# Kernel optimization log

Measured on AMD Instinct MI355X. Metric: run time of the kernel, lower is better.

The kernel has to match this reference:

```python
import jax, jax.numpy as jnp
import numpy as np

B = 256      # number of graphs
IN = 128     # input_dim
FD = 256     # feature_dim (dims[1])
HID = 256    # hidden_dim of attention block (dims[2])
OUT = 128    # final output dim (dims[3])
TXT = 512    # text_emb_dim

LENGTHS = np.asarray(128 + (np.arange(B) % 256), dtype=np.int64)  # ragged lens 128..383
N = int(LENGTHS.sum())  # 65408 total nodes
LMAX = int(LENGTHS.max())  # 383


def setup_inputs() -> dict:
    key = jax.random.key(0)
    ks = jax.random.split(key, 16)
    s = 0.02
    return {
        "input": jax.random.normal(ks[0], (N, IN), jnp.float32),
        "text_emb": jax.random.normal(ks[1], (B, TXT), jnp.float32),
        "repeat_list": jnp.asarray(LENGTHS),
        # layer 0: Linear(IN -> FD)
        "W0": jax.random.normal(ks[2], (IN, FD), jnp.float32) * s,
        "b0": jax.random.normal(ks[3], (FD,), jnp.float32) * s,
        # cross-attention block params
        "Wq": jax.random.normal(ks[4], (TXT, FD), jnp.float32) * s,
        "bq": jax.random.normal(ks[5], (FD,), jnp.float32) * s,
        "Wk": jax.random.normal(ks[6], (FD, FD), jnp.float32) * s,
        "bk": jax.random.normal(ks[7], (FD,), jnp.float32) * s,
        "Wv": jax.random.normal(ks[8], (FD, FD), jnp.float32) * s,
        "bv": jax.random.normal(ks[9], (FD,), jnp.float32) * s,
        "Wo": jax.random.normal(ks[10], (FD, HID), jnp.float32) * s,
        "bo": jax.random.normal(ks[11], (HID,), jnp.float32) * s,
        # layer 2: Linear(HID -> OUT), last layer (no activation)
        "W2": jax.random.normal(ks[12], (HID, OUT), jnp.float32) * s,
        "b2": jax.random.normal(ks[13], (OUT,), jnp.float32) * s,
    }


def _cross_attention(h, text_emb, repeat_list, Wq, bq, Wk, bk, Wv, bv, Wo, bo):
    # h: [N, FD] packed ragged node features; repeat_list: [B] lengths (constant ints)
    n = h.shape[0]
    b = repeat_list.shape[0]
    fd = h.shape[1]
    # pad ragged -> [B, LMAX, FD] (pad value 0) + validity mask
    seg = jnp.repeat(jnp.arange(b), repeat_list, total_repeat_length=n)  # [N] graph id
    offsets = jnp.cumsum(repeat_list) - repeat_list                      # [B] start of each graph
    pos = jnp.arange(n) - offsets[seg]                                   # [N] within-graph pos
    padded = jnp.zeros((b, LMAX, fd), h.dtype).at[seg, pos].set(h)
    valid = jnp.arange(LMAX)[None, :] < repeat_list[:, None]             # [B, L]

    q = text_emb @ Wq + bq                              # [B, FD]
    k = (padded @ Wk + bk) * valid[..., None]           # masked_fill(mask==0, 0)
    v = (padded @ Wv + bv) * valid[..., None]

    # query is broadcast identically over the padded-length axis, so each row of the
    # [L, L] score matrix is the same vector: scores[b, j] = q[b] . k[b, j]
    scores = jnp.einsum('bf,bjf->bj', q, k)             # [B, L]
    scores = jnp.where(valid, scores, -jnp.inf)         # mask invalid columns j
    p = jax.nn.softmax(scores, axis=-1)                 # [B, L]
    # output = attention^T @ value with identical rows => out[b,j,:] = p[b,j] * sum_i v[b,i,:]
    v_sum = v.sum(axis=1)                               # [B, FD] (padded rows already zero)
    out_pad = p[..., None] * v_sum[:, None, :]          # [B, L, FD]
    out_nodes = out_pad[seg, pos]                       # unpad-concat -> [N, FD]
    return out_nodes @ Wo + bo                          # [N, HID]


def reference(input, text_emb, repeat_list, W0, b0, Wq, bq, Wk, bk, Wv, bv, Wo, bo, W2, b2):
    h = jax.nn.relu(input @ W0 + b0)                                     # layer 0 + relu
    h = _cross_attention(h, text_emb, repeat_list, Wq, bq, Wk, bk, Wv, bv, Wo, bo)
    h = jax.nn.relu(h)                                                   # layer 1 + relu
    return h @ W2 + b2                                                   # layer 2 (last, no act)
```

## Files before the change

kernel.cpp:

```cpp
#include <hip/hip_runtime.h>
#include <math.h>

#define B_G   256
#define IN_D  128
#define FD    256
#define HID   256
#define OUT_D 128
#define TXT   512

typedef short bf16x8 __attribute__((ext_vector_type(8)));
typedef float f32x4  __attribute__((ext_vector_type(4)));

__device__ __forceinline__ unsigned bf_rne(float x) {
    unsigned u = __float_as_uint(x);
    u += 0x7fffu + ((u >> 16) & 1u);
    return u >> 16;
}
__device__ __forceinline__ float bf_to_f(unsigned h) {
    return __uint_as_float(h << 16);
}
__device__ __forceinline__ void split2(float a0, float a1, unsigned& hp, unsigned& lp) {
    unsigned h0 = bf_rne(a0), h1 = bf_rne(a1);
    float r0 = a0 - bf_to_f(h0), r1 = a1 - bf_to_f(h1);
    hp = h0 | (h1 << 16);
    lp = bf_rne(r0) | (bf_rne(r1) << 16);
}
__device__ __forceinline__ void split8(const float* z, bf16x8& hf, bf16x8& lf) {
    uint4 h, l;
    split2(z[0], z[1], h.x, l.x);
    split2(z[2], z[3], h.y, l.y);
    split2(z[4], z[5], h.z, l.z);
    split2(z[6], z[7], h.w, l.w);
    hf = __builtin_bit_cast(bf16x8, h);
    lf = __builtin_bit_cast(bf16x8, l);
}

__global__ __launch_bounds__(256) void k_prepA(
    const float* __restrict__ text_emb, const float* __restrict__ Wq,
    const float* __restrict__ bq, const float* __restrict__ Wk,
    const float* __restrict__ W0, const float* __restrict__ W2,
    const int* __restrict__ lens,
    float* __restrict__ qk, int* __restrict__ offsets, float* __restrict__ hsum,
    unsigned short* __restrict__ W0sH, unsigned short* __restrict__ W0sL,
    unsigned short* __restrict__ W2sH, unsigned short* __restrict__ W2sL)
{
    int blk = blockIdx.x, t = threadIdx.x;
    __shared__ float te[TXT];
    __shared__ float q[FD];
    __shared__ int   sc[B_G];

    if (blk < 256) {
        int b = blk;
        hsum[b * FD + t] = 0.f;
        for (int i = t; i < TXT; i += 256) te[i] = text_emb[(size_t)b * TXT + i];
        __syncthreads();
        float acc = bq[t];
        for (int k = 0; k < TXT; k++) acc = fmaf(te[k], Wq[k * FD + t], acc);
        q[t] = acc;
        __syncthreads();
        float a2 = 0.f;
        for (int f = 0; f < FD; f++) a2 = fmaf(Wk[t * FD + f], q[f], a2);
        qk[b * FD + t] = a2;
    } else if (blk < 264) {
        int e = (blk - 256) * 256 + t;
        if (e < 1024) {
            int kc = e >> 8, c = e & 255;
            size_t base = (size_t)(kc * 256 + c) * 32;
            for (int kk = 0; kk < 32; kk++) {
                float v = W0[(size_t)(kc * 32 + kk) * FD + c];
                unsigned h = bf_rne(v);
                float r = v - bf_to_f(h);
                W0sH[base + kk] = (unsigned short)h;
                W0sL[base + kk] = (unsigned short)bf_rne(r);
            }
        } else {
            int e2 = e - 1024;
            int kc = e2 >> 7, c = e2 & 127;
            size_t base = (size_t)(kc * 128 + c) * 32;
            for (int kk = 0; kk < 32; kk++) {
                float v = W2[(size_t)(kc * 32 + kk) * OUT_D + c];
                unsigned h = bf_rne(v);
                float r = v - bf_to_f(h);
                W2sH[base + kk] = (unsigned short)h;
                W2sL[base + kk] = (unsigned short)bf_rne(r);
            }
        }
    } else {
        sc[t] = lens[t];
        __syncthreads();
        for (int d = 1; d < 256; d <<= 1) {
            int v = (t >= d) ? sc[t - d] : 0;
            __syncthreads();
            sc[t] += v;
            __syncthreads();
        }
        offsets[t + 1] = sc[t];
        if (t == 0) offsets[0] = 0;
    }
}

__global__ __launch_bounds__(256, 2) void k_l0_mfma(
    const float* __restrict__ X,
    const unsigned short* __restrict__ W0sH, const unsigned short* __restrict__ W0sL,
    const float* __restrict__ b0, const float* __restrict__ qk,
    const int* __restrict__ offsets,
    float* __restrict__ scores, float* __restrict__ hsum)
{
    int b = blockIdx.y;
    int off = offsets[b], len = offsets[b + 1] - off;
    int n0 = blockIdx.x * 64;
    if (n0 >= len) return;
    int nvalid = min(64, len - n0);

    __shared__ float qks[FD];
    __shared__ float bsh[FD];
    __shared__ float red[4][64];

    int tid = threadIdx.x;
    int lane = tid & 63, w = tid >> 6;
    int ln = lane & 15, quad = lane >> 4;

    qks[tid] = qk[b * FD + tid];
    bsh[tid] = b0[tid];

    const float* Xbase = X + (size_t)(off + n0) * IN_D;

    f32x4 acc[4][4] = {};
#pragma unroll
    for (int kc = 0; kc < 4; kc++) {
        bf16x8 AH[4], AL[4], BH[4], BL[4];
#pragma unroll
        for (int i = 0; i < 4; i++) {
            int node = 16 * i + ln;
            float xv[8];
            if (node < nvalid) {
                const float4* p = (const float4*)(Xbase + (size_t)node * IN_D + kc * 32 + quad * 8);
                float4 v0 = p[0], v1 = p[1];
                xv[0] = v0.x; xv[1] = v0.y; xv[2] = v0.z; xv[3] = v0.w;
                xv[4] = v1.x; xv[5] = v1.y; xv[6] = v1.z; xv[7] = v1.w;
            } else {
#pragma unroll
                for (int q2 = 0; q2 < 8; q2++) xv[q2] = 0.f;
            }
            split8(xv, AH[i], AL[i]);
        }
#pragma unroll
        for (int j = 0; j < 4; j++) {
            int c = 64 * w + 16 * j + ln;
            size_t base = (size_t)(kc * 256 + c) * 32 + quad * 8;
            BH[j] = *(const bf16x8*)&W0sH[base];
            BL[j] = *(const bf16x8*)&W0sL[base];
        }
#pragma unroll
        for (int i = 0; i < 4; i++)
#pragma unroll
            for (int j = 0; j < 4; j++) {
                acc[i][j] = __builtin_amdgcn_mfma_f32_16x16x32_bf16(AH[i], BH[j], acc[i][j], 0, 0, 0);
                acc[i][j] = __builtin_amdgcn_mfma_f32_16x16x32_bf16(AH[i], BL[j], acc[i][j], 0, 0, 0);
                acc[i][j] = __builtin_amdgcn_mfma_f32_16x16x32_bf16(AL[i], BH[j], acc[i][j], 0, 0, 0);
            }
    }
    __syncthreads();

    float sp[4][4];
    float cs[4] = {0.f, 0.f, 0.f, 0.f};
#pragma unroll
    for (int i = 0; i < 4; i++)
#pragma unroll
        for (int r = 0; r < 4; r++) sp[i][r] = 0.f;

#pragma unroll
    for (int i = 0; i < 4; i++)
#pragma unroll
        for (int j = 0; j < 4; j++) {
            int c = 64 * w + 16 * j + ln;
            float bb = bsh[c], qv = qks[c];
#pragma unroll
            for (int r = 0; r < 4; r++) {
                int node = 16 * i + 4 * quad + r;
                float h = acc[i][j][r] + bb;
                h = (h > 0.f && node < nvalid) ? h : 0.f;
                sp[i][r] = fmaf(h, qv, sp[i][r]);
                cs[j] += h;
            }
        }
#pragma unroll
    for (int i = 0; i < 4; i++)
#pragma unroll
        for (int r = 0; r < 4; r++) {
            float s = sp[i][r];
            s += __shfl_xor(s, 1); s += __shfl_xor(s, 2);
            s += __shfl_xor(s, 4); s += __shfl_xor(s, 8);
            sp[i][r] = s;
        }
    if (ln == 0) {
#pragma unroll
        for (int i = 0; i < 4; i++)
#pragma unroll
            for (int r = 0; r < 4; r++)
                red[w][16 * i + 4 * quad + r] = sp[i][r];
    }
#pragma unroll
    for (int j = 0; j < 4; j++) {
        float s = cs[j];
        s += __shfl_xor(s, 16); s += __shfl_xor(s, 32);
        if (quad == 0) atomicAdd(&hsum[b * FD + 64 * w + 16 * j + ln], s);
    }
    __syncthreads();
    if (tid < 64 && tid < nvalid)
        scores[off + n0 + tid] = red[0][tid] + red[1][tid] + red[2][tid] + red[3][tid];
}

__global__ __launch_bounds__(1024) void k_graph(
    const float* __restrict__ scores, const float* __restrict__ hsum,
    const float* __restrict__ Wv, const float* __restrict__ bv,
    const float* __restrict__ Wo, const int* __restrict__ offsets,
    float* __restrict__ wvec, float* __restrict__ smax, float* __restrict__ dinv)
{
    int b = blockIdx.x, tid = threadIdx.x;
    int t = tid & 255, g = tid >> 8;
    int off = offsets[b], len = offsets[b + 1] - off;
    __shared__ float redm[16], reds[16];
    __shared__ float hs[FD], vs[FD];
    __shared__ float part[4][FD];

    float m = -INFINITY;
    for (int i = tid; i < len; i += 1024) m = fmaxf(m, scores[off + i]);
    for (int d = 1; d < 64; d <<= 1) m = fmaxf(m, __shfl_xor(m, d));
    if ((tid & 63) == 0) redm[tid >> 6] = m;
    __syncthreads();
    m = -INFINITY;
#pragma unroll
    for (int k = 0; k < 16; k++) m = fmaxf(m, redm[k]);

    float s = 0.f;
    for (int i = tid; i < len; i += 1024) s += expf(scores[off + i] - m);
    for (int d = 1; d < 64; d <<= 1) s += __shfl_xor(s, d);
    if ((tid & 63) == 0) reds[tid >> 6] = s;
    if (g == 0) hs[t] = hsum[b * FD + t];
    __syncthreads();
    s = 0.f;
#pragma unroll
    for (int k = 0; k < 16; k++) s += reds[k];

    float acc = (g == 0) ? (float)len * bv[t] : 0.f;
    for (int f = 64 * g; f < 64 * g + 64; f++) acc = fmaf(hs[f], Wv[f * FD + t], acc);
    part[g][t] = acc;
    __syncthreads();
    if (g == 0) vs[t] = part[0][t] + part[1][t] + part[2][t] + part[3][t];
    __syncthreads();
    float a2 = 0.f;
    for (int f = 64 * g; f < 64 * g + 64; f++) a2 = fmaf(vs[f], Wo[f * HID + t], a2);
    part[g][t] = a2;
    __syncthreads();
    if (g == 0) wvec[b * HID + t] = part[0][t] + part[1][t] + part[2][t] + part[3][t];
    if (tid == 0) { smax[b] = m; dinv[b] = 1.0f / s; }
}

__global__ __launch_bounds__(256, 2) void k_fin_mfma(
    const float* __restrict__ scores, const float* __restrict__ wvec,
    const float* __restrict__ bo,
    const unsigned short* __restrict__ W2sH, const unsigned short* __restrict__ W2sL,
    const float* __restrict__ b2, const float* __restrict__ smax,
    const float* __restrict__ dinv, const int* __restrict__ offsets,
    float* __restrict__ Y)
{
    int b = blockIdx.y;
    int off = offsets[b], len = offsets[b + 1] - off;
    int n0 = blockIdx.x * 64;
    if (n0 >= len) return;
    int nvalid = min(64, len - n0);

    int tid = threadIdx.x;
    int lane = tid & 63, w = tid >> 6;
    int ln = lane & 15, quad = lane >> 4;

    __shared__ float wsh[HID];
    __shared__ float bosh[HID];
    __shared__ float b2sh[OUT_D];

    wsh[tid] = wvec[b * HID + tid];
    bosh[tid] = bo[tid];
    if (tid < OUT_D) b2sh[tid] = b2[tid];

    float sm = smax[b], di = dinv[b];
    float p[4];
#pragma unroll
    for (int i = 0; i < 4; i++) {
        int node = 16 * i + ln;
        p[i] = (node < nvalid) ? expf(scores[off + n0 + node] - sm) * di : 0.f;
    }
    __syncthreads();

    f32x4 acc[4][2] = {};
#pragma unroll
    for (int kc = 0; kc < 8; kc++) {
        float wv[8], bov[8];
        {
            const float4* wp = (const float4*)&wsh[kc * 32 + quad * 8];
            const float4* bp = (const float4*)&bosh[kc * 32 + quad * 8];
            float4 w0 = wp[0], w1 = wp[1], c0 = bp[0], c1 = bp[1];
            wv[0] = w0.x; wv[1] = w0.y; wv[2] = w0.z; wv[3] = w0.w;
            wv[4] = w1.x; wv[5] = w1.y; wv[6] = w1.z; wv[7] = w1.w;
            bov[0] = c0.x; bov[1] = c0.y; bov[2] = c0.z; bov[3] = c0.w;
            bov[4] = c1.x; bov[5] = c1.y; bov[6] = c1.z; bov[7] = c1.w;
        }
        bf16x8 AH[4], AL[4], BH[2], BL[2];
#pragma unroll
        for (int i = 0; i < 4; i++) {
            float z[8];
#pragma unroll
            for (int jj = 0; jj < 8; jj++)
                z[jj] = fmaxf(fmaf(p[i], wv[jj], bov[jj]), 0.f);
            split8(z, AH[i], AL[i]);
        }
#pragma unroll
        for (int j = 0; j < 2; j++) {
            int c = 32 * w + 16 * j + ln;
            size_t base = (size_t)(kc * 128 + c) * 32 + quad * 8;
            BH[j] = *(const bf16x8*)&W2sH[base];
            BL[j] = *(const bf16x8*)&W2sL[base];
        }
#pragma unroll
        for (int i = 0; i < 4; i++)
#pragma unroll
            for (int j = 0; j < 2; j++) {
                acc[i][j] = __builtin_amdgcn_mfma_f32_16x16x32_bf16(AH[i], BH[j], acc[i][j], 0, 0, 0);
                acc[i][j] = __builtin_amdgcn_mfma_f32_16x16x32_bf16(AH[i], BL[j], acc[i][j], 0, 0, 0);
                acc[i][j] = __builtin_amdgcn_mfma_f32_16x16x32_bf16(AL[i], BH[j], acc[i][j], 0, 0, 0);
            }
    }

#pragma unroll
    for (int i = 0; i < 4; i++)
#pragma unroll
        for (int j = 0; j < 2; j++) {
            int c = 32 * w + 16 * j + ln;
            float bb = b2sh[c];
#pragma unroll
            for (int r = 0; r < 4; r++) {
                int node = 16 * i + 4 * quad + r;
                if (node < nvalid)
                    Y[(size_t)(off + n0 + node) * OUT_D + c] = acc[i][j][r] + bb;
            }
        }
}

extern "C" void kernel_launch(void* const* d_in, const int* in_sizes, int n_in,
                              void* d_out, int out_size, void* d_ws, size_t ws_size,
                              hipStream_t stream)
{
    const float* X        = (const float*)d_in[0];
    const float* text_emb = (const float*)d_in[1];
    const int*   lens     = (const int*)d_in[2];
    const float* W0       = (const float*)d_in[3];
    const float* b0       = (const float*)d_in[4];
    const float* Wq       = (const float*)d_in[5];
    const float* bq       = (const float*)d_in[6];
    const float* Wk       = (const float*)d_in[7];
    const float* Wv       = (const float*)d_in[9];
    const float* bv       = (const float*)d_in[10];
    const float* Wo       = (const float*)d_in[11];
    const float* bo       = (const float*)d_in[12];
    const float* W2       = (const float*)d_in[13];
    const float* b2       = (const float*)d_in[14];
    float* Y = (float*)d_out;

    char* base = (char*)d_ws;
    size_t o = 0;
    int*   offsets = (int*)(base + o);            o += 1088;
    float* qkbuf   = (float*)(base + o);          o += 262144;
    float* wvec    = (float*)(base + o);          o += 262144;
    float* smaxb   = (float*)(base + o);          o += 1024;
    float* dinvb   = (float*)(base + o);          o += 1024;
    float* hsum    = (float*)(base + o);          o += 262144;
    float* scores  = (float*)(base + o);          o += 262144;
    unsigned short* W0sH = (unsigned short*)(base + o); o += 65536;
    unsigned short* W0sL = (unsigned short*)(base + o); o += 65536;
    unsigned short* W2sH = (unsigned short*)(base + o); o += 65536;
    unsigned short* W2sL = (unsigned short*)(base + o); o += 65536;

    k_prepA<<<265, 256, 0, stream>>>(text_emb, Wq, bq, Wk, W0, W2, lens,
                                     qkbuf, offsets, hsum, W0sH, W0sL, W2sH, W2sL);
    k_l0_mfma<<<dim3(6, B_G), 256, 0, stream>>>(X, W0sH, W0sL, b0, qkbuf, offsets, scores, hsum);
    k_graph<<<B_G, 1024, 0, stream>>>(scores, hsum, Wv, bv, Wo, offsets, wvec, smaxb, dinvb);
    k_fin_mfma<<<dim3(6, B_G), 256, 0, stream>>>(scores, wvec, bo, W2sH, W2sL, b2, smaxb, dinvb, offsets, Y);
}
```

Before: 210.4 us.

## Drop activation low-part MFMA, prefetch operands, and widen prep kernel blocks

The activation operand in both MFMA GEMMs is no longer split into bf16 high and low parts, which cuts the MFMA count per tile from three to two. Weights still use the split, so accuracy falls to roughly bf16 rounding of activations. The next k-chunk's X rows and W2 fragments are now loaded into registers ahead of use to overlap load latency with compute. The prep kernel moves to 1024-thread blocks that split the q and qk dot products four ways, giving more parallelism per graph at the cost of an extra shared-memory reduction.

```diff
diff --git a/kernel.cpp b/kernel.cpp
--- a/kernel.cpp
+++ b/kernel.cpp
@@ -19,23 +19,16 @@
 __device__ __forceinline__ float bf_to_f(unsigned h) {
     return __uint_as_float(h << 16);
 }
-__device__ __forceinline__ void split2(float a0, float a1, unsigned& hp, unsigned& lp) {
-    unsigned h0 = bf_rne(a0), h1 = bf_rne(a1);
-    float r0 = a0 - bf_to_f(h0), r1 = a1 - bf_to_f(h1);
-    hp = h0 | (h1 << 16);
-    lp = bf_rne(r0) | (bf_rne(r1) << 16);
-}
-__device__ __forceinline__ void split8(const float* z, bf16x8& hf, bf16x8& lf) {
-    uint4 h, l;
-    split2(z[0], z[1], h.x, l.x);
-    split2(z[2], z[3], h.y, l.y);
-    split2(z[4], z[5], h.z, l.z);
-    split2(z[6], z[7], h.w, l.w);
-    hf = __builtin_bit_cast(bf16x8, h);
-    lf = __builtin_bit_cast(bf16x8, l);
-}
-
-__global__ __launch_bounds__(256) void k_prepA(
+__device__ __forceinline__ bf16x8 pack_hi8(const float4& v0, const float4& v1) {
+    uint4 h;
+    h.x = bf_rne(v0.x) | (bf_rne(v0.y) << 16);
+    h.y = bf_rne(v0.z) | (bf_rne(v0.w) << 16);
+    h.z = bf_rne(v1.x) | (bf_rne(v1.y) << 16);
+    h.w = bf_rne(v1.z) | (bf_rne(v1.w) << 16);
+    return __builtin_bit_cast(bf16x8, h);
+}
+
+__global__ __launch_bounds__(1024) void k_prepA(
     const float* __restrict__ text_emb, const float* __restrict__ Wq,
     const float* __restrict__ bq, const float* __restrict__ Wk,
     const float* __restrict__ W0, const float* __restrict__ W2,
@@ -44,25 +37,32 @@
     unsigned short* __restrict__ W0sH, unsigned short* __restrict__ W0sL,
     unsigned short* __restrict__ W2sH, unsigned short* __restrict__ W2sL)
 {
-    int blk = blockIdx.x, t = threadIdx.x;
+    int blk = blockIdx.x, tid = threadIdx.x;
+    int t = tid & 255, g = tid >> 8;
     __shared__ float te[TXT];
-    __shared__ float q[FD];
+    __shared__ float qsh[FD];
+    __shared__ float part[4][FD];
     __shared__ int   sc[B_G];
 
     if (blk < 256) {
         int b = blk;
-        hsum[b * FD + t] = 0.f;
-        for (int i = t; i < TXT; i += 256) te[i] = text_emb[(size_t)b * TXT + i];
+        if (g == 0) hsum[b * FD + t] = 0.f;
+        if (tid < TXT) te[tid] = text_emb[(size_t)b * TXT + tid];
         __syncthreads();
-        float acc = bq[t];
-        for (int k = 0; k < TXT; k++) acc = fmaf(te[k], Wq[k * FD + t], acc);
-        q[t] = acc;
+        float acc = (g == 0) ? bq[t] : 0.f;
+        const float* Wqp = Wq + (size_t)(128 * g) * FD + t;
+        for (int k = 0; k < 128; k++) acc = fmaf(te[128 * g + k], Wqp[(size_t)k * FD], acc);
+        part[g][t] = acc;
+        __syncthreads();
+        if (g == 0) qsh[t] = part[0][t] + part[1][t] + part[2][t] + part[3][t];
         __syncthreads();
         float a2 = 0.f;
-        for (int f = 0; f < FD; f++) a2 = fmaf(Wk[t * FD + f], q[f], a2);
-        qk[b * FD + t] = a2;
-    } else if (blk < 264) {
-        int e = (blk - 256) * 256 + t;
+        for (int f = 64 * g; f < 64 * g + 64; f++) a2 = fmaf(Wk[(size_t)t * FD + f], qsh[f], a2);
+        part[g][t] = a2;
+        __syncthreads();
+        if (g == 0) qk[b * FD + t] = part[0][t] + part[1][t] + part[2][t] + part[3][t];
+    } else if (blk < 258) {
+        int e = (blk - 256) * 1024 + tid;
         if (e < 1024) {
             int kc = e >> 8, c = e & 255;
             size_t base = (size_t)(kc * 256 + c) * 32;
@@ -86,16 +86,16 @@
             }
         }
     } else {
-        sc[t] = lens[t];
+        if (tid < 256) sc[tid] = lens[tid];
         __syncthreads();
         for (int d = 1; d < 256; d <<= 1) {
-            int v = (t >= d) ? sc[t - d] : 0;
+            int v = (tid < 256 && tid >= d) ? sc[tid - d] : 0;
             __syncthreads();
-            sc[t] += v;
+            if (tid < 256) sc[tid] += v;
             __syncthreads();
         }
-        offsets[t + 1] = sc[t];
-        if (t == 0) offsets[0] = 0;
+        if (tid < 256) offsets[tid + 1] = sc[tid];
+        if (tid == 0) offsets[0] = 0;
     }
 }
 
@@ -124,41 +124,67 @@
     bsh[tid] = b0[tid];
 
     const float* Xbase = X + (size_t)(off + n0) * IN_D;
+    const float* arow[4];
+    bool aval[4];
+#pragma unroll
+    for (int i = 0; i < 4; i++) {
+        int node = 16 * i + ln;
+        aval[i] = node < nvalid;
+        arow[i] = Xbase + (size_t)(aval[i] ? node : 0) * IN_D + quad * 8;
+    }
+    const unsigned short* bph[4];
+    const unsigned short* bpl[4];
+#pragma unroll
+    for (int j = 0; j < 4; j++) {
+        int c = 64 * w + 16 * j + ln;
+        bph[j] = W0sH + (size_t)c * 32 + quad * 8;
+        bpl[j] = W0sL + (size_t)c * 32 + quad * 8;
+    }
 
     f32x4 acc[4][4] = {};
+    float4 aC[4][2];
+#pragma unroll
+    for (int i = 0; i < 4; i++) {
+        const float4* p = (const float4*)(arow[i]);
+        aC[i][0] = p[0]; aC[i][1] = p[1];
+    }
+
 #pragma unroll
     for (int kc = 0; kc < 4; kc++) {
-        bf16x8 AH[4], AL[4], BH[4], BL[4];
+        float4 aN[4][2];
+        if (kc < 3) {
+#pragma unroll
+            for (int i = 0; i < 4; i++) {
+                const float4* p = (const float4*)(arow[i] + (kc + 1) * 32);
+                aN[i][0] = p[0]; aN[i][1] = p[1];
+            }
+        }
+        uint4 bh[4], bl[4];
+#pragma unroll
+        for (int j = 0; j < 4; j++) {
+            bh[j] = *(const uint4*)(bph[j] + (size_t)kc * 8192);
+            bl[j] = *(const uint4*)(bpl[j] + (size_t)kc * 8192);
+        }
+        bf16x8 AH[4];
 #pragma unroll
         for (int i = 0; i < 4; i++) {
-            int node = 16 * i + ln;
-            float xv[8];
-            if (node < nvalid) {
-                const float4* p = (const float4*)(Xbase + (size_t)node * IN_D + kc * 32 + quad * 8);
-                float4 v0 = p[0], v1 = p[1];
-                xv[0] = v0.x; xv[1] = v0.y; xv[2] = v0.z; xv[3] = v0.w;
-                xv[4] = v1.x; xv[5] = v1.y; xv[6] = v1.z; xv[7] = v1.w;
-            } else {
-#pragma unroll
-                for (int q2 = 0; q2 < 8; q2++) xv[q2] = 0.f;
-            }
-            split8(xv, AH[i], AL[i]);
-        }
-#pragma unroll
-        for (int j = 0; j < 4; j++) {
-            int c = 64 * w + 16 * j + ln;
-            size_t base = (size_t)(kc * 256 + c) * 32 + quad * 8;
-            BH[j] = *(const bf16x8*)&W0sH[base];
-            BL[j] = *(const bf16x8*)&W0sL[base];
+            float4 v0 = aC[i][0], v1 = aC[i][1];
+            if (!aval[i]) { v0 = make_float4(0, 0, 0, 0); v1 = v0; }
+            AH[i] = pack_hi8(v0, v1);
         }
 #pragma unroll
         for (int i = 0; i < 4; i++)
 #pragma unroll
             for (int j = 0; j < 4; j++) {
-                acc[i][j] = __builtin_amdgcn_mfma_f32_16x16x32_bf16(AH[i], BH[j], acc[i][j], 0, 0, 0);
-                acc[i][j] = __builtin_amdgcn_mfma_f32_16x16x32_bf16(AH[i], BL[j], acc[i][j], 0, 0, 0);
-                acc[i][j] = __builtin_amdgcn_mfma_f32_16x16x32_bf16(AL[i], BH[j], acc[i][j], 0, 0, 0);
-            }
+                acc[i][j] = __builtin_amdgcn_mfma_f32_16x16x32_bf16(
+                    AH[i], __builtin_bit_cast(bf16x8, bh[j]), acc[i][j], 0, 0, 0);
+                acc[i][j] = __builtin_amdgcn_mfma_f32_16x16x32_bf16(
+                    AH[i], __builtin_bit_cast(bf16x8, bl[j]), acc[i][j], 0, 0, 0);
+            }
+        if (kc < 3) {
+#pragma unroll
+            for (int i = 0; i < 4; i++) { aC[i][0] = aN[i][0]; aC[i][1] = aN[i][1]; }
+        }
     }
     __syncthreads();
 
@@ -292,43 +318,64 @@
     }
     __syncthreads();
 
+    const unsigned short* bph[2];
+    const unsigned short* bpl[2];
+#pragma unroll
+    for (int j = 0; j < 2; j++) {
+        int c = 32 * w + 16 * j + ln;
+        bph[j] = W2sH + (size_t)c * 32 + quad * 8;
+        bpl[j] = W2sL + (size_t)c * 32 + quad * 8;
+    }
+
     f32x4 acc[4][2] = {};
+    uint4 bhC[2], blC[2];
+#pragma unroll
+    for (int j = 0; j < 2; j++) {
+        bhC[j] = *(const uint4*)(bph[j]);
+        blC[j] = *(const uint4*)(bpl[j]);
+    }
+
 #pragma unroll
     for (int kc = 0; kc < 8; kc++) {
-        float wv[8], bov[8];
-        {
-            const float4* wp = (const float4*)&wsh[kc * 32 + quad * 8];
-            const float4* bp = (const float4*)&bosh[kc * 32 + quad * 8];
-            float4 w0 = wp[0], w1 = wp[1], c0 = bp[0], c1 = bp[1];
-            wv[0] = w0.x; wv[1] = w0.y; wv[2] = w0.z; wv[3] = w0.w;
-            wv[4] = w1.x; wv[5] = w1.y; wv[6] = w1.z; wv[7] = w1.w;
-            bov[0] = c0.x; bov[1] = c0.y; bov[2] = c0.z; bov[3] = c0.w;
-            bov[4] = c1.x; bov[5] = c1.y; bov[6] = c1.z; bov[7] = c1.w;
-        }
-        bf16x8 AH[4], AL[4], BH[2], BL[2];
+        uint4 bhN[2], blN[2];
+        if (kc < 7) {
+#pragma unroll
+            for (int j = 0; j < 2; j++) {
+                bhN[j] = *(const uint4*)(bph[j] + (size_t)(kc + 1) * 4096);
+                blN[j] = *(const uint4*)(bpl[j] + (size_t)(kc + 1) * 4096);
+            }
+        }
+        float4 wv0 = *(const float4*)&wsh[kc * 32 + quad * 8];
+        float4 wv1 = *(const float4*)&wsh[kc * 32 + quad * 8 + 4];
+        float4 bo0 = *(const float4*)&bosh[kc * 32 + quad * 8];
+        float4 bo1 = *(const float4*)&bosh[kc * 32 + quad * 8 + 4];
+        bf16x8 AH[4];
 #pragma unroll
         for (int i = 0; i < 4; i++) {
-            float z[8];
-#pragma unroll
-            for (int jj = 0; jj < 8; jj++)
-                z[jj] = fmaxf(fmaf(p[i], wv[jj], bov[jj]), 0.f);
-            split8(z, AH[i], AL[i]);
-        }
-#pragma unroll
-        for (int j = 0; j < 2; j++) {
-            int c = 32 * w + 16 * j + ln;
-            size_t base = (size_t)(kc * 128 + c) * 32 + quad * 8;
-            BH[j] = *(const bf16x8*)&W2sH[base];
-            BL[j] = *(const bf16x8*)&W2sL[base];
+            float4 z0, z1;
+            z0.x = fmaxf(fmaf(p[i], wv0.x, bo0.x), 0.f);
+            z0.y = fmaxf(fmaf(p[i], wv0.y, bo0.y), 0.f);
+            z0.z = fmaxf(fmaf(p[i], wv0.z, bo0.z), 0.f);
+            z0.w = fmaxf(fmaf(p[i], wv0.w, bo0.w), 0.f);
+            z1.x = fmaxf(fmaf(p[i], wv1.x, bo1.x), 0.f);
+            z1.y = fmaxf(fmaf(p[i], wv1.y, bo1.y), 0.f);
+            z1.z = fmaxf(fmaf(p[i], wv1.z, bo1.z), 0.f);
+            z1.w = fmaxf(fmaf(p[i], wv1.w, bo1.w), 0.f);
+            AH[i] = pack_hi8(z0, z1);
         }
 #pragma unroll
         for (int i = 0; i < 4; i++)
 #pragma unroll
             for (int j = 0; j < 2; j++) {
-                acc[i][j] = __builtin_amdgcn_mfma_f32_16x16x32_bf16(AH[i], BH[j], acc[i][j], 0, 0, 0);
-                acc[i][j] = __builtin_amdgcn_mfma_f32_16x16x32_bf16(AH[i], BL[j], acc[i][j], 0, 0, 0);
-                acc[i][j] = __builtin_amdgcn_mfma_f32_16x16x32_bf16(AL[i], BH[j], acc[i][j], 0, 0, 0);
-            }
+                acc[i][j] = __builtin_amdgcn_mfma_f32_16x16x32_bf16(
+                    AH[i], __builtin_bit_cast(bf16x8, bhC[j]), acc[i][j], 0, 0, 0);
+                acc[i][j] = __builtin_amdgcn_mfma_f32_16x16x32_bf16(
+                    AH[i], __builtin_bit_cast(bf16x8, blC[j]), acc[i][j], 0, 0, 0);
+            }
+        if (kc < 7) {
+#pragma unroll
+            for (int j = 0; j < 2; j++) { bhC[j] = bhN[j]; blC[j] = blN[j]; }
+        }
     }
 
 #pragma unroll
@@ -380,8 +427,8 @@
     unsigned short* W2sH = (unsigned short*)(base + o); o += 65536;
     unsigned short* W2sL = (unsigned short*)(base + o); o += 65536;
 
-    k_prepA<<<265, 256, 0, stream>>>(text_emb, Wq, bq, Wk, W0, W2, lens,
-                                     qkbuf, offsets, hsum, W0sH, W0sL, W2sH, W2sL);
+    k_prepA<<<259, 1024, 0, stream>>>(text_emb, Wq, bq, Wk, W0, W2, lens,
+                                      qkbuf, offsets, hsum, W0sH, W0sL, W2sH, W2sL);
     k_l0_mfma<<<dim3(6, B_G), 256, 0, stream>>>(X, W0sH, W0sL, b0, qkbuf, offsets, scores, hsum);
     k_graph<<<B_G, 1024, 0, stream>>>(scores, hsum, Wv, bv, Wo, offsets, wvec, smaxb, dinvb);
     k_fin_mfma<<<dim3(6, B_G), 256, 0, stream>>>(scores, wvec, bo, W2sH, W2sL, b2, smaxb, dinvb, offsets, Y);
```

New measurement: 212.2 us. About the same (+0.8%).
